# Kernel optimization log

Measured on AMD Instinct MI355X. Metric: run time of the kernel, lower is better.

The kernel has to match this reference:

```python
import jax, jax.numpy as jnp
import numpy as np

B, T, D, H = 16, 4096, 1024, 32
EPS = 1e-6


def setup_inputs() -> dict:
    key = jax.random.key(0)
    ks = jax.random.split(key, 12)
    inp = {
        'Z_real': jax.random.normal(ks[0], (B, T, D), jnp.float32),
        'Z_imag': jax.random.normal(ks[1], (B, T, D), jnp.float32),
        'mask': jnp.ones((B, T), jnp.float32),
        # psi_mag: Linear(1,H) -> GELU -> Linear(H,1)  (xavier gain 0.1, zero bias)
        'W1m': jax.random.normal(ks[2], (H, 1), jnp.float32) * 0.1,
        'b1m': jnp.zeros((H,), jnp.float32),
        'W2m': jax.random.normal(ks[3], (1, H), jnp.float32) * 0.1,
        'b2m': jnp.zeros((1,), jnp.float32),
        # psi_phase: Linear(2,H) -> GELU -> Linear(H,2)
        'W1p': jax.random.normal(ks[4], (H, 2), jnp.float32) * 0.1,
        'b1p': jnp.zeros((H,), jnp.float32),
        'W2p': jax.random.normal(ks[5], (2, H), jnp.float32) * 0.1,
        'b2p': jnp.zeros((2,), jnp.float32),
        'mag_scale': jnp.float32(0.1),
    }
    return inp


def reference(Z_real, Z_imag, mask, W1m, b1m, W2m, b2m, W1p, b1p, W2p, b2p, mag_scale):
    m = mask[:, :, None]  # (B,T,1)
    count = jnp.clip(jnp.sum(m, axis=1, keepdims=True), 1.0)  # (B,1,1)
    Ar = jnp.sum(Z_real * m, axis=1, keepdims=True) / count   # (B,1,D)
    Ai = jnp.sum(Z_imag * m, axis=1, keepdims=True) / count
    mag = jnp.sqrt(Ar * Ar + Ai * Ai)
    log_mag = jnp.log(mag + EPS)                               # (B,1,D)
    phase_vec = jnp.stack([Ar, Ai], axis=-1) / (mag[..., None] + EPS)  # (B,1,D,2)
    # psi_mag on scalar feature
    h = jax.nn.gelu(log_mag[..., None] @ W1m.T + b1m, approximate=False)  # (B,1,D,H)
    mag_delta = (h @ W2m.T + b2m)[..., 0]                      # (B,1,D)
    log_mag_out = log_mag + mag_scale * mag_delta
    # psi_phase on 2-vector
    hp = jax.nn.gelu(phase_vec @ W1p.T + b1p, approximate=False)  # (B,1,D,H)
    pv = hp @ W2p.T + b2p                                      # (B,1,D,2)
    norm = jnp.maximum(jnp.sqrt(jnp.sum(pv * pv, axis=-1, keepdims=True)), 1e-12)
    pv = pv / norm
    r_out = jnp.exp(log_mag_out)
    A_new_r = r_out * pv[..., 0]
    A_new_i = r_out * pv[..., 1]
    out = jnp.stack([Z_real + A_new_r, Z_imag + A_new_i], axis=0)  # (2,B,T,D)
    return out
```

## Files before the change

### kernel.cpp

```cpp
#include <hip/hip_runtime.h>
#include <math.h>

#define BB 16
#define TT 4096
#define DD 1024
#define HH 32

static constexpr float kEPS = 1e-6f;

#define TCHUNK 64
__global__ __launch_bounds__(256) void reduce_kernel(
    const float* __restrict__ zr, const float* __restrict__ zi,
    const float* __restrict__ mask,
    float* __restrict__ arW, float* __restrict__ aiW, float* __restrict__ cntW) {
  const int b = blockIdx.y;
  const int t0 = blockIdx.x * TCHUNK;
  const int tid = threadIdx.x;
  const int d4 = tid * 4;

  float4 accR = make_float4(0.f, 0.f, 0.f, 0.f);
  float4 accI = make_float4(0.f, 0.f, 0.f, 0.f);
  float msum = 0.f;

  const size_t base = ((size_t)b * TT + t0) * DD + d4;
  const float* zrp = zr + base;
  const float* zip = zi + base;
  const float* mp = mask + (size_t)b * TT + t0;

  for (int t = 0; t < TCHUNK; ++t) {
    const float m = mp[t];
    msum += m;
    float4 r = *(const float4*)(zrp + (size_t)t * DD);
    float4 im = *(const float4*)(zip + (size_t)t * DD);
    accR.x += r.x * m; accR.y += r.y * m; accR.z += r.z * m; accR.w += r.w * m;
    accI.x += im.x * m; accI.y += im.y * m; accI.z += im.z * m; accI.w += im.w * m;
  }

  const int o = b * DD + d4;
  atomicAdd(&arW[o + 0], accR.x);
  atomicAdd(&arW[o + 1], accR.y);
  atomicAdd(&arW[o + 2], accR.z);
  atomicAdd(&arW[o + 3], accR.w);
  atomicAdd(&aiW[o + 0], accI.x);
  atomicAdd(&aiW[o + 1], accI.y);
  atomicAdd(&aiW[o + 2], accI.z);
  atomicAdd(&aiW[o + 3], accI.w);
  if (tid == 0) atomicAdd(&cntW[b], msum);
}

__global__ __launch_bounds__(256) void mlp_kernel(
    const float* __restrict__ arW, const float* __restrict__ aiW,
    const float* __restrict__ cntW,
    const float* __restrict__ W1m, const float* __restrict__ b1m,
    const float* __restrict__ W2m, const float* __restrict__ b2m,
    const float* __restrict__ W1p, const float* __restrict__ b1p,
    const float* __restrict__ W2p, const float* __restrict__ b2p,
    const float* __restrict__ mag_scale,
    float* __restrict__ anR, float* __restrict__ anI) {
  const int i = blockIdx.x * blockDim.x + threadIdx.x;
  if (i >= BB * DD) return;
  const int b = i >> 10;

  const float count = fmaxf(cntW[b], 1.0f);
  const float Ar = arW[i] / count;
  const float Ai = aiW[i] / count;
  const float mag = sqrtf(Ar * Ar + Ai * Ai);
  const float log_mag = logf(mag + kEPS);
  const float inv_me = 1.0f / (mag + kEPS);
  const float pr = Ar * inv_me;
  const float pi = Ai * inv_me;

  float md = b2m[0];
  #pragma unroll
  for (int j = 0; j < HH; ++j) {
    float h = log_mag * W1m[j] + b1m[j];
    h = 0.5f * h * (1.0f + erff(h * 0.70710678118654752440f));
    md += h * W2m[j];
  }
  const float lmo = log_mag + mag_scale[0] * md;

  float pv0 = b2p[0];
  float pv1 = b2p[1];
  #pragma unroll
  for (int j = 0; j < HH; ++j) {
    float hp = pr * W1p[2 * j] + pi * W1p[2 * j + 1] + b1p[j];
    hp = 0.5f * hp * (1.0f + erff(hp * 0.70710678118654752440f));
    pv0 += hp * W2p[j];
    pv1 += hp * W2p[HH + j];
  }
  const float nrm = fmaxf(sqrtf(pv0 * pv0 + pv1 * pv1), 1e-12f);
  const float r_out = expf(lmo);
  anR[i] = r_out * pv0 / nrm;
  anI[i] = r_out * pv1 / nrm;
}

__global__ __launch_bounds__(256) void add_kernel(
    const float* __restrict__ zr, const float* __restrict__ zi,
    const float* __restrict__ anR, const float* __restrict__ anI,
    float* __restrict__ out) {
  const size_t N4 = (size_t)BB * TT * DD / 4;
  const size_t stride = (size_t)gridDim.x * blockDim.x;
  float* out0 = out;
  float* out1 = out + (size_t)BB * TT * DD;

  for (size_t i = (size_t)blockIdx.x * blockDim.x + threadIdx.x; i < N4; i += stride) {
    const size_t e = i * 4;
    const int b = (int)(e >> 22);
    const int d = (int)(e & (DD - 1));
    const int o = b * DD + d;
    float4 ar4 = *(const float4*)(anR + o);
    float4 ai4 = *(const float4*)(anI + o);
    float4 r = ((const float4*)zr)[i];
    float4 im = ((const float4*)zi)[i];
    r.x += ar4.x; r.y += ar4.y; r.z += ar4.z; r.w += ar4.w;
    im.x += ai4.x; im.y += ai4.y; im.z += ai4.z; im.w += ai4.w;
    ((float4*)out0)[i] = r;
    ((float4*)out1)[i] = im;
  }
}

extern "C" void kernel_launch(void* const* d_in, const int* in_sizes, int n_in,
                              void* d_out, int out_size, void* d_ws, size_t ws_size,
                              hipStream_t stream) {
  const float* zr = (const float*)d_in[0];
  const float* zi = (const float*)d_in[1];
  const float* mask = (const float*)d_in[2];
  const float* W1m = (const float*)d_in[3];
  const float* b1m = (const float*)d_in[4];
  const float* W2m = (const float*)d_in[5];
  const float* b2m = (const float*)d_in[6];
  const float* W1p = (const float*)d_in[7];
  const float* b1p = (const float*)d_in[8];
  const float* W2p = (const float*)d_in[9];
  const float* b2p = (const float*)d_in[10];
  const float* mag_scale = (const float*)d_in[11];

  float* ws = (float*)d_ws;
  float* arW = ws;
  float* aiW = ws + 16384;
  float* cntW = ws + 32768;
  float* anR = ws + 32800;
  float* anI = ws + 49184;

  hipMemsetAsync(d_ws, 0, (32768 + 32) * sizeof(float), stream);

  dim3 g1(TT / TCHUNK, BB);
  reduce_kernel<<<g1, 256, 0, stream>>>(zr, zi, mask, arW, aiW, cntW);

  mlp_kernel<<<(BB * DD + 255) / 256, 256, 0, stream>>>(
      arW, aiW, cntW, W1m, b1m, W2m, b2m, W1p, b1p, W2p, b2p, mag_scale, anR, anI);

  add_kernel<<<2048, 256, 0, stream>>>(zr, zi, anR, anI, (float*)d_out);
}
```

Measured before the change: 335.5 us.

## Traverse add kernel in reverse order with nontemporal loads/stores for cache reuse

The add kernel now walks its grid-stride loop in reverse (last blocks and iterations first), so the tail of Z that the reduce kernel touched last may still sit in the L2/MALL cache when it is reread. It also switches the streaming loads and stores to nontemporal builtins so the output writes do not evict cached input. The reduce loop is unrolled by four and rewritten with ext_vector_type arithmetic. These rely on cache-residency behaviour, and the nontemporal hints could also bypass useful reuse.

```diff
diff --git a/kernel.cpp b/kernel.cpp
--- a/kernel.cpp
+++ b/kernel.cpp
@@ -7,6 +7,8 @@
 #define HH 32
 
 static constexpr float kEPS = 1e-6f;
+
+typedef float f32x4 __attribute__((ext_vector_type(4)));
 
 #define TCHUNK 64
 __global__ __launch_bounds__(256) void reduce_kernel(
@@ -18,8 +20,8 @@
   const int tid = threadIdx.x;
   const int d4 = tid * 4;
 
-  float4 accR = make_float4(0.f, 0.f, 0.f, 0.f);
-  float4 accI = make_float4(0.f, 0.f, 0.f, 0.f);
+  f32x4 accR = (f32x4)(0.f);
+  f32x4 accI = (f32x4)(0.f);
   float msum = 0.f;
 
   const size_t base = ((size_t)b * TT + t0) * DD + d4;
@@ -27,13 +29,14 @@
   const float* zip = zi + base;
   const float* mp = mask + (size_t)b * TT + t0;
 
+  #pragma unroll 4
   for (int t = 0; t < TCHUNK; ++t) {
     const float m = mp[t];
     msum += m;
-    float4 r = *(const float4*)(zrp + (size_t)t * DD);
-    float4 im = *(const float4*)(zip + (size_t)t * DD);
-    accR.x += r.x * m; accR.y += r.y * m; accR.z += r.z * m; accR.w += r.w * m;
-    accI.x += im.x * m; accI.y += im.y * m; accI.z += im.z * m; accI.w += im.w * m;
+    f32x4 r = *(const f32x4*)(zrp + (size_t)t * DD);
+    f32x4 im = *(const f32x4*)(zip + (size_t)t * DD);
+    accR += r * m;
+    accI += im * m;
   }
 
   const int o = b * DD + d4;
@@ -103,19 +106,25 @@
   float* out0 = out;
   float* out1 = out + (size_t)BB * TT * DD;
 
-  for (size_t i = (size_t)blockIdx.x * blockDim.x + threadIdx.x; i < N4; i += stride) {
+  const int rb = gridDim.x - 1 - blockIdx.x;
+  const size_t lane = (size_t)rb * blockDim.x + threadIdx.x;
+  const long long nIter = (long long)((N4 + stride - 1) / stride);
+
+  for (long long it = nIter - 1; it >= 0; --it) {
+    const size_t i = (size_t)it * stride + lane;
+    if (i >= N4) continue;
     const size_t e = i * 4;
     const int b = (int)(e >> 22);
     const int d = (int)(e & (DD - 1));
     const int o = b * DD + d;
-    float4 ar4 = *(const float4*)(anR + o);
-    float4 ai4 = *(const float4*)(anI + o);
-    float4 r = ((const float4*)zr)[i];
-    float4 im = ((const float4*)zi)[i];
-    r.x += ar4.x; r.y += ar4.y; r.z += ar4.z; r.w += ar4.w;
-    im.x += ai4.x; im.y += ai4.y; im.z += ai4.z; im.w += ai4.w;
-    ((float4*)out0)[i] = r;
-    ((float4*)out1)[i] = im;
+    f32x4 ar4 = *(const f32x4*)(anR + o);
+    f32x4 ai4 = *(const f32x4*)(anI + o);
+    f32x4 r  = __builtin_nontemporal_load((const f32x4*)zr + i);
+    f32x4 im = __builtin_nontemporal_load((const f32x4*)zi + i);
+    r += ar4;
+    im += ai4;
+    __builtin_nontemporal_store(r, (f32x4*)out0 + i);
+    __builtin_nontemporal_store(im, (f32x4*)out1 + i);
   }
 }
 
@@ -142,7 +151,7 @@
   float* anR = ws + 32800;
   float* anI = ws + 49184;
 
-  hipMemsetAsync(d_ws, 0, (32768 + 32) * sizeof(float), stream);
+  (void)hipMemsetAsync(d_ws, 0, (32768 + 32) * sizeof(float), stream);
 
   dim3 g1(TT / TCHUNK, BB);
   reduce_kernel<<<g1, 256, 0, stream>>>(zr, zi, mask, arW, aiW, cntW);
```

New measurement: 313.3 us. -6.6%, faster.
